# Performance work log

Measured on AMD Instinct MI355X. Metric: run time of the kernel, lower is better.

## Reference

```python
import jax, jax.numpy as jnp
import numpy as np

Z = 16384      # batch of points
N_IN = 127     # dim(Rs_in)
N = N_IN + 1   # +1 ones channel since linear=True
K = 128        # dim(Rs_out)
DIM_TS = 2080  # dim(Rs_ts), ~ n(n+1)/2 surviving tensor-square paths
T_DENSITY = 0.05  # CG-like tensor T is sparse


def setup_inputs() -> dict:
    key = jax.random.key(0)
    k1, k2, k3, k4 = jax.random.split(key, 4)
    features = jax.random.normal(k1, (Z, N_IN), dtype=jnp.float32)
    W = jax.random.normal(k2, (K, DIM_TS), dtype=jnp.float32)  # KernelLinear weights
    T = jax.random.normal(k3, (DIM_TS, N * N), dtype=jnp.float32)
    mask = jax.random.uniform(k4, (DIM_TS, N * N)) < T_DENSITY  # emulate sparse CG structure
    T = jnp.where(mask, T, 0.0)
    return {"features": features, "W": W, "T": T}


def reference(features, W, T):
    # features: [Z, n_in]; prepend ones column (linear=True path)
    f = jnp.concatenate(
        [jnp.ones((features.shape[0], 1), dtype=features.dtype), features], axis=1
    )  # [Z, N]
    # kernel = (T.t() @ W.T).T reshaped -> equivalently (W @ T).reshape(K, N, N)
    kernel3 = (W @ T).reshape(K, N, N)
    # out[z,k] = sum_ij kernel3[k,i,j] * f[z,i] * f[z,j]
    return jnp.einsum('kij,zi,zj->zk', kernel3, f, f)
```

## Files before the change

kernel.cpp:

```cpp
#include <hip/hip_runtime.h>


#define ZTOT 16384
#define NIN  127
#define KOUT 128
#define DTS  2080
#define PTOT 16384

typedef _Float16 h8 __attribute__((ext_vector_type(8)));
typedef _Float16 h2 __attribute__((ext_vector_type(2)));
typedef float f32x4 __attribute__((ext_vector_type(4)));
typedef float f32x16 __attribute__((ext_vector_type(16)));

static __device__ __forceinline__ void gl16(const void* g, void* l) {
  __builtin_amdgcn_global_load_lds((const __attribute__((address_space(1))) unsigned int*)g,
                                   (__attribute__((address_space(3))) unsigned int*)l, 16, 0, 0);
}

__global__ __launch_bounds__(256) void k_wf(const float* __restrict__ W,
                                            _Float16* __restrict__ Wf) {
  const int t = threadIdx.x, lane = t & 63;
  const int unit = blockIdx.x * 4 + (t >> 6);
  if (unit >= 520) return;
  const int s = unit >> 3, kg = unit & 7;
  const int krow = kg * 16 + (lane & 15);
  const int dbase = s * 32 + ((lane >> 4) << 3);
  h8 v;
#pragma unroll
  for (int e = 0; e < 8; ++e) v[e] = (_Float16)W[(size_t)krow * DTS + dbase + e];
  *(h8*)(Wf + ((size_t)unit * 64 + lane) * 8) = v;
}

__global__ __launch_bounds__(256, 4) void k_wt(const float* __restrict__ T,
                                               const _Float16* __restrict__ Wf,
                                               _Float16* __restrict__ K3) {
  const int t = threadIdx.x, lane = t & 63, w = t >> 6;
  const int p0 = blockIdx.x * 16;
  const int prow = p0 + (lane & 15);
  const int dg = (lane >> 4) << 3;
  f32x4 acc0 = {}, acc1 = {};
  const _Float16* wf0 = Wf + ((size_t)(w * 2) * 64 + lane) * 8;
#pragma unroll 2
  for (int s = 0; s < 65; ++s) {
    const size_t tb = (size_t)(s * 32 + dg) * PTOT + prow;
    h8 b;
#pragma unroll
    for (int e = 0; e < 8; ++e) b[e] = (_Float16)T[tb + (size_t)e * PTOT];
    const h8 a0 = *(const h8*)(wf0 + (size_t)s * 4096);
    const h8 a1 = *(const h8*)(wf0 + (size_t)s * 4096 + 512);
    acc0 = __builtin_amdgcn_mfma_f32_16x16x32_f16(a0, b, acc0, 0, 0, 0);
    acc1 = __builtin_amdgcn_mfma_f32_16x16x32_f16(a1, b, acc1, 0, 0, 0);
  }
  const int rbase = (lane >> 4) << 2;
#pragma unroll
  for (int r = 0; r < 4; ++r) {
    K3[(size_t)(w * 32 + rbase + r) * PTOT + prow] = (_Float16)acc0[r];
    K3[(size_t)(w * 32 + 16 + rbase + r) * PTOT + prow] = (_Float16)acc1[r];
  }
}

__global__ __launch_bounds__(256, 2) void k_qf(const float* __restrict__ features,
                                               const _Float16* __restrict__ K3,
                                               float* __restrict__ out) {
  __shared__ __align__(16) _Float16 B0[16384];
  __shared__ __align__(16) _Float16 B1[16384];
  __shared__ _Float16 fT[32 * 136];
  const int t = threadIdx.x, lane = t & 63, w = t >> 6;
  const int zg = w >> 1, kg = w & 1, hg = lane >> 5, l31 = lane & 31;
  const int zb = blockIdx.x >> 2, ic = blockIdx.x & 3;
  const int z0 = zb * 128, i0 = ic * 32;

  {
    const int row = t >> 1, hf = t & 1;
    const float* fr = features + (size_t)(z0 + row) * NIN;
    const int rs = (row & 7) << 4;
#pragma unroll
    for (int qb = 0; qb < 8; ++qb) {
      h8 v;
#pragma unroll
      for (int e = 0; e < 8; ++e) {
        const int j = hf * 64 + qb * 8 + e;
        v[e] = (j == 0) ? (_Float16)1.0f : (_Float16)fr[j - 1];
      }
      *(h8*)((char*)B0 + row * 256 + (((hf * 8 + qb) * 16) ^ rs)) = v;
    }
  }
  {
    const int z = t >> 1, ih = t & 1;
#pragma unroll
    for (int q = 0; q < 16; ++q) {
      const int il = ih * 16 + q, gi = i0 + il;
      const float fv = (gi == 0) ? 1.0f : features[(size_t)(z0 + z) * NIN + gi - 1];
      fT[il * 136 + z] = (_Float16)fv;
    }
  }
  __syncthreads();

  h8 fj8[2][8];
#pragma unroll
  for (int m = 0; m < 2; ++m) {
    const int rowm = zg * 64 + m * 32 + l31;
    const int rs = (rowm & 7) << 4;
#pragma unroll
    for (int kc = 0; kc < 8; ++kc)
      fj8[m][kc] = *(const h8*)((const char*)B0 + rowm * 256 + (((kc * 2 + hg) * 16) ^ rs));
  }
  __syncthreads();

  const _Float16* Kbase = K3 + (size_t)i0 * 128;
#define STAGE_B(BUF, IPH)                                                      \
  {                                                                            \
    const _Float16* src = Kbase + (IPH) * 128;                                 \
    _Pragma("unroll") for (int r = 0; r < 8; ++r) {                            \
      const int Lb = r * 4096 + w * 1024;                                      \
      const int row = (Lb >> 8) + (lane >> 4);                                 \
      const int us = (lane & 15) ^ (row & 7);                                  \
      gl16(src + (size_t)row * PTOT + us * 8, (char*)(BUF) + Lb);              \
    }                                                                          \
  }

  f32x16 acc[2][2] = {};
  STAGE_B(B0, 0)
  __syncthreads();

  const int rs0 = (l31 & 7) << 4;
  const int brow0 = (kg * 64 + l31) * 256;
  const int brow1 = (kg * 64 + 32 + l31) * 256;

#define PHASE(CURB, NXTB, PH, DO_STAGE)                                        \
  {                                                                            \
    if (DO_STAGE) STAGE_B(NXTB, (PH) + 1)                                      \
    const _Float16 f0 = fT[(PH) * 136 + zg * 64 + l31];                        \
    const _Float16 f1 = fT[(PH) * 136 + zg * 64 + 32 + l31];                   \
    const h2 fi0 = {f0, f0};                                                   \
    const h2 fi1 = {f1, f1};                                                   \
    _Pragma("unroll") for (int kc = 0; kc < 8; ++kc) {                         \
      const int uoff = ((kc * 2 + hg) * 16) ^ rs0;                             \
      const h8 b0 = *(const h8*)((const char*)(CURB) + brow0 + uoff);          \
      const h8 b1 = *(const h8*)((const char*)(CURB) + brow1 + uoff);          \
      h8 a0, a1;                                                               \
      _Pragma("unroll") for (int r = 0; r < 4; ++r) {                          \
        const h2 j0 = {fj8[0][kc][2 * r], fj8[0][kc][2 * r + 1]};              \
        const h2 j1 = {fj8[1][kc][2 * r], fj8[1][kc][2 * r + 1]};              \
        const h2 p0 = fi0 * j0;                                                \
        const h2 p1 = fi1 * j1;                                                \
        a0[2 * r] = p0[0]; a0[2 * r + 1] = p0[1];                              \
        a1[2 * r] = p1[0]; a1[2 * r + 1] = p1[1];                              \
      }                                                                        \
      acc[0][0] = __builtin_amdgcn_mfma_f32_32x32x16_f16(a0, b0, acc[0][0], 0, 0, 0); \
      acc[0][1] = __builtin_amdgcn_mfma_f32_32x32x16_f16(a0, b1, acc[0][1], 0, 0, 0); \
      acc[1][0] = __builtin_amdgcn_mfma_f32_32x32x16_f16(a1, b0, acc[1][0], 0, 0, 0); \
      acc[1][1] = __builtin_amdgcn_mfma_f32_32x32x16_f16(a1, b1, acc[1][1], 0, 0, 0); \
    }                                                                          \
    __syncthreads();                                                           \
  }

  for (int pb = 0; pb < 16; ++pb) {
    PHASE(B0, B1, pb * 2, true)
    PHASE(B1, B0, pb * 2 + 1, (pb < 15))
  }

  const int kq = kg * 64 + l31;
#pragma unroll
  for (int m = 0; m < 2; ++m)
#pragma unroll
    for (int n = 0; n < 2; ++n)
#pragma unroll
      for (int r = 0; r < 16; ++r) {
        const int zr = (r & 3) + ((r >> 2) << 3) + (hg << 2);
        const int z = z0 + zg * 64 + m * 32 + zr;
        atomicAdd(out + (size_t)z * KOUT + kq + n * 32, acc[m][n][r]);
      }
}

extern "C" void kernel_launch(void* const* d_in, const int* in_sizes, int n_in,
                              void* d_out, int out_size, void* d_ws, size_t ws_size,
                              hipStream_t stream) {
  const float* features = (const float*)d_in[0];
  const float* W        = (const float*)d_in[1];
  const float* T        = (const float*)d_in[2];
  float* out = (float*)d_out;
  _Float16* K3h = (_Float16*)d_ws;
  _Float16* Wf  = (_Float16*)d_out;

  k_wf<<<dim3(130), dim3(256), 0, stream>>>(W, Wf);
  k_wt<<<dim3(1024), dim3(256), 0, stream>>>(T, Wf, K3h);
  hipMemsetAsync(d_out, 0, (size_t)ZTOT * KOUT * sizeof(float), stream);
  k_qf<<<dim3(512), dim3(256), 0, stream>>>(features, K3h, out);
}
```

Measured before the change: 339.8 us.

## Split W@T reduction across two blocks with register prefetch and fp16 sum

The W·T kernel now splits the 65-step reduction over D into even and odd halves, each computed by its own block, which doubles the grid. Each block writes partial fp16 results into the output buffer, and a new elementwise kernel sums the two halves into the workspace. The loop also software-prefetches the next step's T and W fragments into registers, and the occupancy hint is raised to 6. This is meant to expose more parallelism and latency hiding on the strided T loads, at the cost of an extra kernel launch, an extra pass over the partials, and fp16 rounding of each partial sum.

```diff
diff --git a/kernel.cpp b/kernel.cpp
--- a/kernel.cpp
+++ b/kernel.cpp
@@ -31,25 +31,52 @@
   *(h8*)(Wf + ((size_t)unit * 64 + lane) * 8) = v;
 }
 
-__global__ __launch_bounds__(256, 4) void k_wt(const float* __restrict__ T,
+__global__ __launch_bounds__(256, 6) void k_wt(const float* __restrict__ T,
                                                const _Float16* __restrict__ Wf,
-                                               _Float16* __restrict__ K3) {
+                                               _Float16* __restrict__ K3p) {
   const int t = threadIdx.x, lane = t & 63, w = t >> 6;
-  const int p0 = blockIdx.x * 16;
+  const int ptile = blockIdx.x >> 1, dh = blockIdx.x & 1;
+  const int p0 = ptile * 16;
   const int prow = p0 + (lane & 15);
   const int dg = (lane >> 4) << 3;
+  _Float16* K3 = K3p + (size_t)dh * (128 * PTOT);
+  const _Float16* wf0 = Wf + (size_t)w * 1024 + (size_t)lane * 8;
+
   f32x4 acc0 = {}, acc1 = {};
-  const _Float16* wf0 = Wf + ((size_t)(w * 2) * 64 + lane) * 8;
-#pragma unroll 2
-  for (int s = 0; s < 65; ++s) {
-    const size_t tb = (size_t)(s * 32 + dg) * PTOT + prow;
+  float fc[8];
+  h8 ac0, ac1;
+  {
+    const size_t tb = (size_t)(dh * 32 + dg) * PTOT + prow;
+#pragma unroll
+    for (int e = 0; e < 8; ++e) fc[e] = T[tb + (size_t)e * PTOT];
+    ac0 = *(const h8*)(wf0 + (size_t)dh * 4096);
+    ac1 = *(const h8*)(wf0 + (size_t)dh * 4096 + 512);
+  }
+  int s = dh;
+  for (; s + 2 < 65; s += 2) {
+    float fn[8];
+    h8 an0, an1;
+    const int sn = s + 2;
+    const size_t tb = (size_t)(sn * 32 + dg) * PTOT + prow;
+#pragma unroll
+    for (int e = 0; e < 8; ++e) fn[e] = T[tb + (size_t)e * PTOT];
+    an0 = *(const h8*)(wf0 + (size_t)sn * 4096);
+    an1 = *(const h8*)(wf0 + (size_t)sn * 4096 + 512);
     h8 b;
 #pragma unroll
-    for (int e = 0; e < 8; ++e) b[e] = (_Float16)T[tb + (size_t)e * PTOT];
-    const h8 a0 = *(const h8*)(wf0 + (size_t)s * 4096);
-    const h8 a1 = *(const h8*)(wf0 + (size_t)s * 4096 + 512);
-    acc0 = __builtin_amdgcn_mfma_f32_16x16x32_f16(a0, b, acc0, 0, 0, 0);
-    acc1 = __builtin_amdgcn_mfma_f32_16x16x32_f16(a1, b, acc1, 0, 0, 0);
+    for (int e = 0; e < 8; ++e) b[e] = (_Float16)fc[e];
+    acc0 = __builtin_amdgcn_mfma_f32_16x16x32_f16(ac0, b, acc0, 0, 0, 0);
+    acc1 = __builtin_amdgcn_mfma_f32_16x16x32_f16(ac1, b, acc1, 0, 0, 0);
+#pragma unroll
+    for (int e = 0; e < 8; ++e) fc[e] = fn[e];
+    ac0 = an0; ac1 = an1;
+  }
+  {
+    h8 b;
+#pragma unroll
+    for (int e = 0; e < 8; ++e) b[e] = (_Float16)fc[e];
+    acc0 = __builtin_amdgcn_mfma_f32_16x16x32_f16(ac0, b, acc0, 0, 0, 0);
+    acc1 = __builtin_amdgcn_mfma_f32_16x16x32_f16(ac1, b, acc1, 0, 0, 0);
   }
   const int rbase = (lane >> 4) << 2;
 #pragma unroll
@@ -57,6 +84,15 @@
     K3[(size_t)(w * 32 + rbase + r) * PTOT + prow] = (_Float16)acc0[r];
     K3[(size_t)(w * 32 + 16 + rbase + r) * PTOT + prow] = (_Float16)acc1[r];
   }
+}
+
+__global__ __launch_bounds__(256) void k_sum(const _Float16* __restrict__ A,
+                                             const _Float16* __restrict__ B,
+                                             _Float16* __restrict__ O) {
+  const size_t i = ((size_t)blockIdx.x * 256 + threadIdx.x) * 8;
+  const h8 a = *(const h8*)(A + i);
+  const h8 b = *(const h8*)(B + i);
+  *(h8*)(O + i) = a + b;
 }
 
 __global__ __launch_bounds__(256, 2) void k_qf(const float* __restrict__ features,
@@ -180,11 +216,15 @@
   const float* W        = (const float*)d_in[1];
   const float* T        = (const float*)d_in[2];
   float* out = (float*)d_out;
+
   _Float16* K3h = (_Float16*)d_ws;
-  _Float16* Wf  = (_Float16*)d_out;
+  _Float16* Wf  = K3h + (size_t)2 * 1024 * 1024;
+  _Float16* K3a = (_Float16*)d_out;
+  _Float16* K3b = K3a + (size_t)2 * 1024 * 1024;
 
   k_wf<<<dim3(130), dim3(256), 0, stream>>>(W, Wf);
-  k_wt<<<dim3(1024), dim3(256), 0, stream>>>(T, Wf, K3h);
+  k_wt<<<dim3(2048), dim3(256), 0, stream>>>(T, Wf, K3a);
+  k_sum<<<dim3(1024), dim3(256), 0, stream>>>(K3a, K3b, K3h);
   hipMemsetAsync(d_out, 0, (size_t)ZTOT * KOUT * sizeof(float), stream);
   k_qf<<<dim3(512), dim3(256), 0, stream>>>(features, K3h, out);
 }
```

Measured after the change: 353.6 us. 1.04x slower.

## Restructure W@T kernel with LDS-staged coalesced T tiles and split-K reduction

Applied to the files above, without the earlier changes.

The W@T precompute now loads T with coalesced float4 reads, converts it to fp16 and stages it in double-buffered, swizzled shared memory. Each block handles 64 output columns, which improves W-fragment reuse across four MFMA tiles. The reduction dimension is split into two chunks written to separate buffers in d_out, and a new k_sum kernel adds them. This targets the strided, uncoalesced T reads of the old version, at the cost of an extra kernel launch and extra K3 traffic.

```diff
diff --git a/kernel.cpp b/kernel.cpp
--- a/kernel.cpp
+++ b/kernel.cpp
@@ -15,6 +15,10 @@
 static __device__ __forceinline__ void gl16(const void* g, void* l) {
   __builtin_amdgcn_global_load_lds((const __attribute__((address_space(1))) unsigned int*)g,
                                    (__attribute__((address_space(3))) unsigned int*)l, 16, 0, 0);
+}
+
+static __device__ __forceinline__ unsigned int pk16(float a, float b) {
+  return __builtin_bit_cast(unsigned int, __builtin_amdgcn_cvt_pkrtz(a, b));
 }
 
 __global__ __launch_bounds__(256) void k_wf(const float* __restrict__ W,
@@ -31,32 +35,89 @@
   *(h8*)(Wf + ((size_t)unit * 64 + lane) * 8) = v;
 }
 
-__global__ __launch_bounds__(256, 4) void k_wt(const float* __restrict__ T,
+__global__ __launch_bounds__(256, 2) void k_wt(const float* __restrict__ T,
                                                const _Float16* __restrict__ Wf,
-                                               _Float16* __restrict__ K3) {
+                                               _Float16* __restrict__ K3a,
+                                               _Float16* __restrict__ K3b) {
+  __shared__ __align__(16) _Float16 Tb0[64 * 32];
+  __shared__ __align__(16) _Float16 Tb1[64 * 32];
   const int t = threadIdx.x, lane = t & 63, w = t >> 6;
-  const int p0 = blockIdx.x * 16;
-  const int prow = p0 + (lane & 15);
-  const int dg = (lane >> 4) << 3;
-  f32x4 acc0 = {}, acc1 = {};
-  const _Float16* wf0 = Wf + ((size_t)(w * 2) * 64 + lane) * 8;
-#pragma unroll 2
-  for (int s = 0; s < 65; ++s) {
-    const size_t tb = (size_t)(s * 32 + dg) * PTOT + prow;
-    h8 b;
-#pragma unroll
-    for (int e = 0; e < 8; ++e) b[e] = (_Float16)T[tb + (size_t)e * PTOT];
-    const h8 a0 = *(const h8*)(wf0 + (size_t)s * 4096);
-    const h8 a1 = *(const h8*)(wf0 + (size_t)s * 4096 + 512);
-    acc0 = __builtin_amdgcn_mfma_f32_16x16x32_f16(a0, b, acc0, 0, 0, 0);
-    acc1 = __builtin_amdgcn_mfma_f32_16x16x32_f16(a1, b, acc1, 0, 0, 0);
-  }
-  const int rbase = (lane >> 4) << 2;
-#pragma unroll
-  for (int r = 0; r < 4; ++r) {
-    K3[(size_t)(w * 32 + rbase + r) * PTOT + prow] = (_Float16)acc0[r];
-    K3[(size_t)(w * 32 + 16 + rbase + r) * PTOT + prow] = (_Float16)acc1[r];
-  }
+  const int ptile = (int)blockIdx.x >> 1, chunk = (int)blockIdx.x & 1;
+  const int p0 = ptile * 64;
+  const int sb = chunk ? 33 : 0, ns = chunk ? 32 : 33;
+  _Float16* K3c = chunk ? K3b : K3a;
+
+  const int p4 = t & 15, dp = 2 * (t >> 4);
+  const int wbase = 256 * p4 + 16 * ((dp >> 3) ^ (p4 & 3)) + 2 * (dp & 7);
+  const int l15 = lane & 15;
+  const int su = 16 * ((lane >> 4) ^ (l15 >> 2));
+
+  const float* gT = T + (size_t)(sb * 32 + dp) * PTOT + p0 + 4 * p4;
+
+#define LOADW(Q0, Q1, S)                                      \
+  {                                                           \
+    const float* gp = gT + (size_t)(S) * (32 * PTOT);         \
+    Q0 = *(const float4*)gp;                                  \
+    Q1 = *(const float4*)(gp + PTOT);                         \
+  }
+#define WRITEW(BUF, Q0, Q1)                                   \
+  {                                                           \
+    char* wb = (char*)(BUF) + wbase;                          \
+    *(unsigned int*)(wb + 0)   = pk16(Q0.x, Q1.x);            \
+    *(unsigned int*)(wb + 64)  = pk16(Q0.y, Q1.y);            \
+    *(unsigned int*)(wb + 128) = pk16(Q0.z, Q1.z);            \
+    *(unsigned int*)(wb + 192) = pk16(Q0.w, Q1.w);            \
+  }
+#define COMPUTEW(BUF, SG)                                                         \
+  {                                                                               \
+    const _Float16* wfp = Wf + (size_t)(SG) * 4096 + w * 1024 + (size_t)lane * 8; \
+    const h8 a0 = *(const h8*)wfp;                                                \
+    const h8 a1 = *(const h8*)(wfp + 512);                                        \
+    _Pragma("unroll") for (int nf = 0; nf < 4; ++nf) {                            \
+      const h8 b = *(const h8*)((const char*)(BUF) + 64 * (nf * 16 + l15) + su);  \
+      acc0[nf] = __builtin_amdgcn_mfma_f32_16x16x32_f16(a0, b, acc0[nf], 0, 0, 0); \
+      acc1[nf] = __builtin_amdgcn_mfma_f32_16x16x32_f16(a1, b, acc1[nf], 0, 0, 0); \
+    }                                                                             \
+  }
+
+  f32x4 acc0[4] = {}, acc1[4] = {};
+  float4 A0, A1, Br0, Br1;
+  LOADW(A0, A1, 0)
+  LOADW(Br0, Br1, 1)
+  WRITEW(Tb0, A0, A1)
+  __syncthreads();
+  for (int s = 0; s < ns; s += 2) {
+    if (s + 2 < ns) LOADW(A0, A1, s + 2)
+    if (s + 1 < ns) WRITEW(Tb1, Br0, Br1)
+    COMPUTEW(Tb0, sb + s)
+    __syncthreads();
+    if (s + 1 < ns) {
+      if (s + 3 < ns) LOADW(Br0, Br1, s + 3)
+      if (s + 2 < ns) WRITEW(Tb0, A0, A1)
+      COMPUTEW(Tb1, sb + s + 1)
+      __syncthreads();
+    }
+  }
+  const int rb = (lane >> 4) << 2;
+#pragma unroll
+  for (int nf = 0; nf < 4; ++nf)
+#pragma unroll
+    for (int r = 0; r < 4; ++r) {
+      K3c[(size_t)(w * 32 + rb + r) * PTOT + p0 + nf * 16 + l15] = (_Float16)acc0[nf][r];
+      K3c[(size_t)(w * 32 + 16 + rb + r) * PTOT + p0 + nf * 16 + l15] = (_Float16)acc1[nf][r];
+    }
+#undef LOADW
+#undef WRITEW
+#undef COMPUTEW
+}
+
+__global__ __launch_bounds__(256) void k_sum(const _Float16* __restrict__ A,
+                                             const _Float16* __restrict__ B,
+                                             _Float16* __restrict__ O) {
+  const size_t i = ((size_t)blockIdx.x * 256 + threadIdx.x) * 8;
+  const h8 a = *(const h8*)(A + i);
+  const h8 b = *(const h8*)(B + i);
+  *(h8*)(O + i) = a + b;
 }
 
 __global__ __launch_bounds__(256, 2) void k_qf(const float* __restrict__ features,
@@ -180,11 +241,15 @@
   const float* W        = (const float*)d_in[1];
   const float* T        = (const float*)d_in[2];
   float* out = (float*)d_out;
+
   _Float16* K3h = (_Float16*)d_ws;
-  _Float16* Wf  = (_Float16*)d_out;
+  _Float16* Wf  = K3h + (size_t)2 * 1024 * 1024;
+  _Float16* K3a = (_Float16*)d_out;
+  _Float16* K3b = K3a + (size_t)2 * 1024 * 1024;
 
   k_wf<<<dim3(130), dim3(256), 0, stream>>>(W, Wf);
-  k_wt<<<dim3(1024), dim3(256), 0, stream>>>(T, Wf, K3h);
-  hipMemsetAsync(d_out, 0, (size_t)ZTOT * KOUT * sizeof(float), stream);
+  k_wt<<<dim3(512), dim3(256), 0, stream>>>(T, Wf, K3a, K3b);
+  k_sum<<<dim3(1024), dim3(256), 0, stream>>>(K3a, K3b, K3h);
+  (void)hipMemsetAsync(d_out, 0, (size_t)ZTOT * KOUT * sizeof(float), stream);
   k_qf<<<dim3(512), dim3(256), 0, stream>>>(features, K3h, out);
 }
```

New measurement: 289.6 us. 14.8% less time.
